# Optimization experiments

Measured on AMD Instinct MI355X. Metric: run time of the kernel, lower is better.

Reference implementation:

```python
import jax, jax.numpy as jnp
import numpy as np

B, CK, CQ, CV, CO, H, W = 4, 256, 256, 256, 64, 24, 24


def setup_inputs() -> dict:
    key = jax.random.key(0)
    ks = jax.random.split(key, 9)
    s = lambda k, shape, fan: jax.random.normal(k, shape, jnp.float32) * (fan ** -0.5)
    return {
        "key": jax.random.normal(ks[0], (B, CK, H, W), jnp.float32),
        "query": jax.random.normal(ks[1], (B, CQ, H, W), jnp.float32),
        "value": jax.random.normal(ks[2], (B, CV, H, W), jnp.float32),
        "Wk": s(ks[3], (CO, CK), CK),   # 1x1 conv weight for key transform
        "bk": jnp.zeros((CO,), jnp.float32),
        "Wq": s(ks[4], (CO, CQ), CQ),   # 1x1 conv weight for query transform
        "bq": jnp.zeros((CO,), jnp.float32),
        "wf": s(ks[5], (CO,), CO),      # channel-flattening 1x1 conv (CO -> 1)
        "bf": jnp.zeros((), jnp.float32),
    }


def reference(key, query, value, Wk, bk, Wq, bq, wf, bf):
    b, _, hq, wq = query.shape
    nk = key.shape[2] * key.shape[3]
    nq = hq * wq
    # 1x1 conv == per-pixel linear; flatten spatial to (B, N, CO)
    k_ = jnp.einsum('bchw,oc->bhwo', key, Wk).reshape(b, nk, -1) + bk
    q_ = jnp.einsum('bchw,oc->bhwo', query, Wq).reshape(b, nq, -1) + bq
    # broadcast add: (B, Nk, 1, CO) + (B, 1, Nq, CO) -> tanh -> reduce channels
    pre = jnp.tanh(k_[:, :, None, :] + q_[:, None, :, :])
    scores = jnp.einsum('bkqc,c->bkq', pre, wf) + bf
    attn = jax.nn.sigmoid(scores)                      # (B, Nk, Nq)
    v_ = value.reshape(b, value.shape[1], nk)          # (B, CV, Nk)
    out = jnp.einsum('bkq,bck->bcq', attn, v_)         # (B, CV, Nq)
    return out.reshape(b, value.shape[1], hq, wq)
```

## Files before the change

kernel.cpp:

```cpp
#include <hip/hip_runtime.h>
#include <hip/hip_bf16.h>

#define BB 4
#define CIN 256
#define CO 64
#define NN 576
#define NKC 18
#define NQT 36

typedef __attribute__((ext_vector_type(8))) short short8;
typedef __attribute__((ext_vector_type(4))) float floatx4;

__device__ __forceinline__ unsigned short f2bf(float f) {
    unsigned int u = __float_as_uint(f);
    unsigned int r = (u + 0x7fffu + ((u >> 16) & 1u)) >> 16;
    return (unsigned short)r;
}

__global__ void transpose_kernel(const float* __restrict__ key,
                                 const float* __restrict__ query,
                                 float* __restrict__ kt,
                                 float* __restrict__ qt) {
    int z = blockIdx.z;
    const float* src = (z < BB) ? key : query;
    float* dst       = (z < BB) ? kt  : qt;
    int b = z & (BB - 1);
    __shared__ float tile[32][33];
    int n0 = blockIdx.x * 32, c0 = blockIdx.y * 32;
    int tx = threadIdx.x, ty = threadIdx.y;
    const float* s = src + (size_t)b * CIN * NN;
    #pragma unroll
    for (int j = 0; j < 4; ++j) {
        int c = c0 + ty + j * 8;
        tile[ty + j * 8][tx] = s[(size_t)c * NN + n0 + tx];
    }
    __syncthreads();
    float* d = dst + (size_t)b * NN * CIN;
    #pragma unroll
    for (int j = 0; j < 4; ++j) {
        int n = n0 + ty + j * 8;
        d[(size_t)n * CIN + c0 + tx] = tile[tx][ty + j * 8];
    }
}

#define NT 4
__global__ void proj_exp_kernel(const float* __restrict__ kt,
                                const float* __restrict__ qt,
                                const float* __restrict__ Wk, const float* __restrict__ bk,
                                const float* __restrict__ Wq, const float* __restrict__ bq,
                                float* __restrict__ ek, float* __restrict__ eq) {
    int z = blockIdx.z;
    const float* xt   = z ? qt : kt;
    const float* W    = z ? Wq : Wk;
    const float* bias = z ? bq : bk;
    float* outp       = z ? eq : ek;
    int b  = blockIdx.y;
    int n0 = blockIdx.x * NT;
    int o  = threadIdx.x;

    float acc[NT];
    float bv = bias[o];
    #pragma unroll
    for (int i = 0; i < NT; ++i) acc[i] = bv;

    const float* wrow  = W + (size_t)o * CIN;
    const float* xbase = xt + ((size_t)b * NN + n0) * CIN;

    for (int c0 = 0; c0 < CIN; c0 += 64) {
        float4 w[16];
        #pragma unroll
        for (int i = 0; i < 16; ++i) w[i] = ((const float4*)(wrow + c0))[i];
        #pragma unroll
        for (int n = 0; n < NT; ++n) {
            const float* xr = xbase + (size_t)n * CIN + c0;
            #pragma unroll
            for (int i = 0; i < 16; ++i) {
                float4 wv = w[i];
                acc[n] = fmaf(wv.x, xr[4 * i + 0], acc[n]);
                acc[n] = fmaf(wv.y, xr[4 * i + 1], acc[n]);
                acc[n] = fmaf(wv.z, xr[4 * i + 2], acc[n]);
                acc[n] = fmaf(wv.w, xr[4 * i + 3], acc[n]);
            }
        }
    }
    float* op = outp + ((size_t)b * NN + n0) * CO + o;
    #pragma unroll
    for (int i = 0; i < NT; ++i) op[(size_t)i * CO] = __expf(2.0f * acc[i]);
}

__global__ void packv_kernel(const float* __restrict__ value,
                             unsigned short* __restrict__ Vp) {
    int ct = blockIdx.x, kc = blockIdx.y, b = blockIdx.z;
    int l = threadIdx.x;
    int c = ct * 16 + (l & 15);
    int k = kc * 32 + (l >> 4) * 8;
    const float4* src = (const float4*)(value + ((size_t)b * CIN + c) * NN + k);
    float4 v0 = src[0], v1 = src[1];
    uint4 o;
    o.x = (unsigned)f2bf(v0.x) | ((unsigned)f2bf(v0.y) << 16);
    o.y = (unsigned)f2bf(v0.z) | ((unsigned)f2bf(v0.w) << 16);
    o.z = (unsigned)f2bf(v1.x) | ((unsigned)f2bf(v1.y) << 16);
    o.w = (unsigned)f2bf(v1.z) | ((unsigned)f2bf(v1.w) << 16);
    *(uint4*)(Vp + (((size_t)b * 16 + ct) * NKC + kc) * 1024 + l * 8) = o;
}

__global__ void __launch_bounds__(256, 3)
attn_pack_kernel(const float* __restrict__ ek,
                 const float* __restrict__ eq,
                 const float* __restrict__ wf,
                 const float* __restrict__ bfp,
                 unsigned short* __restrict__ Bp) {
    int b  = blockIdx.z;
    int k0 = blockIdx.y * 32;
    int q0 = blockIdx.x * 64;
    int t  = threadIdx.x;
    int l  = t & 63;
    int w  = __builtin_amdgcn_readfirstlane(t >> 6);

    float4 eqv[16], w2v[16];
    const float4* eqp = (const float4*)(eq + ((size_t)b * NN + q0 + l) * CO);
    const float4* wfp = (const float4*)wf;
    float C = bfp[0];
    #pragma unroll
    for (int i = 0; i < 16; ++i) {
        eqv[i] = eqp[i];
        float4 wv = wfp[i];
        C += wv.x + wv.y + wv.z + wv.w;
        wv.x *= 2.0f; wv.y *= 2.0f; wv.z *= 2.0f; wv.w *= 2.0f;
        w2v[i] = wv;
    }

    __shared__ float sc[32][64];

    #pragma unroll 1
    for (int kk = 0; kk < 8; ++kk) {
        int k = k0 + w * 8 + kk;
        const float4* ekr = (const float4*)(ek + ((size_t)b * NN + k) * CO);
        float a0 = 0.f, a1 = 0.f, a2 = 0.f, a3 = 0.f;
        #pragma unroll
        for (int i = 0; i < 16; ++i) {
            float4 k4 = ekr[i];
            float4 e4 = eqv[i];
            float4 w4 = w2v[i];
            a0 = fmaf(w4.x, __builtin_amdgcn_rcpf(fmaf(k4.x, e4.x, 1.0f)), a0);
            a1 = fmaf(w4.y, __builtin_amdgcn_rcpf(fmaf(k4.y, e4.y, 1.0f)), a1);
            a2 = fmaf(w4.z, __builtin_amdgcn_rcpf(fmaf(k4.z, e4.z, 1.0f)), a2);
            a3 = fmaf(w4.w, __builtin_amdgcn_rcpf(fmaf(k4.w, e4.w, 1.0f)), a3);
        }
        float score = C - (a0 + a1) - (a2 + a3);
        float sg = __builtin_amdgcn_rcpf(1.0f + __expf(-score));
        sc[w * 8 + kk][l] = sg;
    }
    __syncthreads();

    int col = w * 16 + (l & 15);
    int row = (l >> 4) * 8;
    uint4 o;
    o.x = (unsigned)f2bf(sc[row + 0][col]) | ((unsigned)f2bf(sc[row + 1][col]) << 16);
    o.y = (unsigned)f2bf(sc[row + 2][col]) | ((unsigned)f2bf(sc[row + 3][col]) << 16);
    o.z = (unsigned)f2bf(sc[row + 4][col]) | ((unsigned)f2bf(sc[row + 5][col]) << 16);
    o.w = (unsigned)f2bf(sc[row + 6][col]) | ((unsigned)f2bf(sc[row + 7][col]) << 16);
    size_t qt = (size_t)blockIdx.x * 4 + w;
    *(uint4*)(Bp + (((size_t)b * NQT + qt) * NKC + blockIdx.y) * 1024 + l * 8) = o;
}

__global__ void av_mfma_kernel(const unsigned short* __restrict__ Vp,
                               const unsigned short* __restrict__ Bp,
                               float* __restrict__ out) {
    int b  = blockIdx.z;
    int ct = blockIdx.y;
    int qx = blockIdx.x;
    int t  = threadIdx.x;
    int l  = t & 63;
    int w  = __builtin_amdgcn_readfirstlane(t >> 6);

    floatx4 acc[4] = {{0.f,0.f,0.f,0.f},{0.f,0.f,0.f,0.f},
                      {0.f,0.f,0.f,0.f},{0.f,0.f,0.f,0.f}};

    const unsigned short* abase = Vp + ((size_t)b * 16 + ct) * NKC * 1024 + l * 8;
    const unsigned short* bbase = Bp + ((size_t)b * NQT + (size_t)qx * 4) * NKC * 1024 + l * 8;

    for (int kc = w; kc < NKC; kc += 4) {
        short8 a = *(const short8*)(abase + (size_t)kc * 1024);
        #pragma unroll
        for (int qt = 0; qt < 4; ++qt) {
            short8 bq = *(const short8*)(bbase + ((size_t)qt * NKC + kc) * 1024);
            acc[qt] = __builtin_amdgcn_mfma_f32_16x16x32_bf16(a, bq, acc[qt], 0, 0, 0);
        }
    }

    __shared__ float red[4][64][17];
    #pragma unroll
    for (int qt = 0; qt < 4; ++qt)
        #pragma unroll
        for (int r = 0; r < 4; ++r)
            red[w][l][qt * 4 + r] = acc[qt][r];
    __syncthreads();

    int q = qx * 64 + w * 16 + (l & 15);
    #pragma unroll
    for (int r = 0; r < 4; ++r) {
        float s = red[0][l][w * 4 + r] + red[1][l][w * 4 + r]
                + red[2][l][w * 4 + r] + red[3][l][w * 4 + r];
        int c = ct * 16 + (l >> 4) * 4 + r;
        out[((size_t)b * CIN + c) * NN + q] = s;
    }
}

extern "C" void kernel_launch(void* const* d_in, const int* in_sizes, int n_in,
                              void* d_out, int out_size, void* d_ws, size_t ws_size,
                              hipStream_t stream) {
    const float* key   = (const float*)d_in[0];
    const float* query = (const float*)d_in[1];
    const float* value = (const float*)d_in[2];
    const float* Wk    = (const float*)d_in[3];
    const float* bk    = (const float*)d_in[4];
    const float* Wq    = (const float*)d_in[5];
    const float* bq    = (const float*)d_in[6];
    const float* wf    = (const float*)d_in[7];
    const float* bf    = (const float*)d_in[8];
    float* out = (float*)d_out;

    float* ws = (float*)d_ws;
    float* ek = ws;
    float* eq = ek + (size_t)BB * NN * CO;
    float* bp_region = eq + (size_t)BB * NN * CO;
    unsigned short* Bp = (unsigned short*)bp_region;
    float* kt = bp_region;
    float* qt = kt + (size_t)BB * NN * CIN;
    unsigned short* Vp = (unsigned short*)(bp_region + 1327104);

    dim3 gt(NN / 32, CIN / 32, 2 * BB);
    transpose_kernel<<<gt, dim3(32, 8), 0, stream>>>(key, query, kt, qt);

    dim3 gp(NN / NT, BB, 2);
    proj_exp_kernel<<<gp, 64, 0, stream>>>(kt, qt, Wk, bk, Wq, bq, ek, eq);

    dim3 gv(16, NKC, BB);
    packv_kernel<<<gv, 64, 0, stream>>>(value, Vp);

    dim3 ga(NN / 64, NN / 32, BB);
    attn_pack_kernel<<<ga, 256, 0, stream>>>(ek, eq, wf, bf, Bp);

    dim3 gm(NN / 64, 16, BB);
    av_mfma_kernel<<<gm, 256, 0, stream>>>(Vp, Bp, out);
}
```

Before: 116.8 us.

## Fuse packing kernels and move 1x1 projections onto bf16 MFMA

The separate transpose, value-pack and weight handling steps are merged into one pack_all kernel. It converts key, query, value and both weight matrices to bf16 MFMA fragment layout in a single launch. The scalar fp32 projection kernel is replaced with a bf16 MFMA 16x16x32 GEMM, and the attention kernel now stages eq through padded shared memory with coalesced loads. Packed buffer strides shrink from 1024 to 512 elements, which removes padding waste. The projections lose precision by moving from fp32 to bf16 inputs, and the exp(2x) step can amplify those errors.

```diff
diff --git a/kernel.cpp b/kernel.cpp
--- a/kernel.cpp
+++ b/kernel.cpp
@@ -6,6 +6,7 @@
 #define CO 64
 #define NN 576
 #define NKC 18
+#define NMT 36
 #define NQT 36
 
 typedef __attribute__((ext_vector_type(8))) short short8;
@@ -17,99 +18,127 @@
     return (unsigned short)r;
 }
 
-__global__ void transpose_kernel(const float* __restrict__ key,
-                                 const float* __restrict__ query,
-                                 float* __restrict__ kt,
-                                 float* __restrict__ qt) {
-    int z = blockIdx.z;
-    const float* src = (z < BB) ? key : query;
-    float* dst       = (z < BB) ? kt  : qt;
-    int b = z & (BB - 1);
+__global__ void __launch_bounds__(256) pack_all(
+    const float* __restrict__ key, const float* __restrict__ query,
+    const float* __restrict__ value,
+    const float* __restrict__ Wk, const float* __restrict__ Wq,
+    unsigned short* __restrict__ Xp, unsigned short* __restrict__ Wp,
+    unsigned short* __restrict__ Vp)
+{
     __shared__ float tile[32][33];
-    int n0 = blockIdx.x * 32, c0 = blockIdx.y * 32;
-    int tx = threadIdx.x, ty = threadIdx.y;
-    const float* s = src + (size_t)b * CIN * NN;
-    #pragma unroll
-    for (int j = 0; j < 4; ++j) {
-        int c = c0 + ty + j * 8;
-        tile[ty + j * 8][tx] = s[(size_t)c * NN + n0 + tx];
-    }
-    __syncthreads();
-    float* d = dst + (size_t)b * NN * CIN;
-    #pragma unroll
-    for (int j = 0; j < 4; ++j) {
-        int n = n0 + ty + j * 8;
-        d[(size_t)n * CIN + c0 + tx] = tile[tx][ty + j * 8];
-    }
-}
-
-#define NT 4
-__global__ void proj_exp_kernel(const float* __restrict__ kt,
-                                const float* __restrict__ qt,
-                                const float* __restrict__ Wk, const float* __restrict__ bk,
-                                const float* __restrict__ Wq, const float* __restrict__ bq,
-                                float* __restrict__ ek, float* __restrict__ eq) {
-    int z = blockIdx.z;
-    const float* xt   = z ? qt : kt;
-    const float* W    = z ? Wq : Wk;
+    int bid = blockIdx.x;
+    int t = threadIdx.x;
+    int l = t & 63;
+    int w = t >> 6;
+
+    if (bid < 1152) {
+        int zb  = bid / 144;
+        int r   = bid % 144;
+        int n32 = r % 18;
+        int kc  = r / 18;
+        int z = zb >> 2, b = zb & 3;
+        const float* src = z ? query : key;
+        int tx = t & 31, ty = t >> 5;
+        const float* s = src + ((size_t)b * CIN + (size_t)kc * 32) * NN + n32 * 32;
+        #pragma unroll
+        for (int j = 0; j < 4; ++j) {
+            int cl = ty + j * 8;
+            tile[cl][tx] = s[(size_t)cl * NN + tx];
+        }
+        __syncthreads();
+        if (w < 2) {
+            int nl = w * 16 + (l & 15);
+            int cl = (l >> 4) * 8;
+            uint4 o;
+            o.x = (unsigned)f2bf(tile[cl + 0][nl]) | ((unsigned)f2bf(tile[cl + 1][nl]) << 16);
+            o.y = (unsigned)f2bf(tile[cl + 2][nl]) | ((unsigned)f2bf(tile[cl + 3][nl]) << 16);
+            o.z = (unsigned)f2bf(tile[cl + 4][nl]) | ((unsigned)f2bf(tile[cl + 5][nl]) << 16);
+            o.w = (unsigned)f2bf(tile[cl + 6][nl]) | ((unsigned)f2bf(tile[cl + 7][nl]) << 16);
+            int mt = n32 * 2 + w;
+            *(uint4*)(Xp + ((((size_t)z * BB + b) * NMT + mt) * 8 + kc) * 512 + l * 8) = o;
+        }
+    } else if (bid < 1168) {
+        int funit = (bid - 1152) * 4 + w;
+        int z  = funit >> 5;
+        int nt = (funit >> 3) & 3;
+        int kc = funit & 7;
+        const float* W = z ? Wq : Wk;
+        int o = nt * 16 + (l & 15);
+        int c = kc * 32 + (l >> 4) * 8;
+        const float4* p = (const float4*)(W + (size_t)o * CIN + c);
+        float4 v0 = p[0], v1 = p[1];
+        uint4 u;
+        u.x = (unsigned)f2bf(v0.x) | ((unsigned)f2bf(v0.y) << 16);
+        u.y = (unsigned)f2bf(v0.z) | ((unsigned)f2bf(v0.w) << 16);
+        u.z = (unsigned)f2bf(v1.x) | ((unsigned)f2bf(v1.y) << 16);
+        u.w = (unsigned)f2bf(v1.z) | ((unsigned)f2bf(v1.w) << 16);
+        *(uint4*)(Wp + (((size_t)z * 4 + nt) * 8 + kc) * 512 + l * 8) = u;
+    } else {
+        int funit = (bid - 1168) * 4 + w;
+        int b  = funit / 288;
+        int r  = funit % 288;
+        int ct = r / 18;
+        int kc = r % 18;
+        int c = ct * 16 + (l & 15);
+        int k = kc * 32 + (l >> 4) * 8;
+        const float4* p = (const float4*)(value + ((size_t)b * CIN + c) * NN + k);
+        float4 v0 = p[0], v1 = p[1];
+        uint4 u;
+        u.x = (unsigned)f2bf(v0.x) | ((unsigned)f2bf(v0.y) << 16);
+        u.y = (unsigned)f2bf(v0.z) | ((unsigned)f2bf(v0.w) << 16);
+        u.z = (unsigned)f2bf(v1.x) | ((unsigned)f2bf(v1.y) << 16);
+        u.w = (unsigned)f2bf(v1.z) | ((unsigned)f2bf(v1.w) << 16);
+        *(uint4*)(Vp + (((size_t)b * 16 + ct) * NKC + kc) * 512 + l * 8) = u;
+    }
+}
+
+__global__ void __launch_bounds__(256) proj_exp_mfma(
+    const unsigned short* __restrict__ Xp, const unsigned short* __restrict__ Wp,
+    const float* __restrict__ bk, const float* __restrict__ bq,
+    float* __restrict__ ek, float* __restrict__ eq)
+{
+    int t = threadIdx.x, l = t & 63, w = t >> 6;
+    int gw = blockIdx.x * 4 + w;
+    int z  = gw / 144;
+    int r  = gw % 144;
+    int b  = r / NMT;
+    int mt = r % NMT;
+
+    const unsigned short* ab = Xp + ((((size_t)z * BB + b) * NMT + mt) * 8) * 512 + l * 8;
+    const unsigned short* wb = Wp + (size_t)z * 32 * 512 + l * 8;
+
+    floatx4 acc[4] = {{0.f,0.f,0.f,0.f},{0.f,0.f,0.f,0.f},
+                      {0.f,0.f,0.f,0.f},{0.f,0.f,0.f,0.f}};
+    #pragma unroll
+    for (int kc = 0; kc < 8; ++kc) {
+        short8 a = *(const short8*)(ab + (size_t)kc * 512);
+        #pragma unroll
+        for (int nt = 0; nt < 4; ++nt) {
+            short8 bf8 = *(const short8*)(wb + ((size_t)nt * 8 + kc) * 512);
+            acc[nt] = __builtin_amdgcn_mfma_f32_16x16x32_bf16(a, bf8, acc[nt], 0, 0, 0);
+        }
+    }
+
     const float* bias = z ? bq : bk;
     float* outp       = z ? eq : ek;
-    int b  = blockIdx.y;
-    int n0 = blockIdx.x * NT;
-    int o  = threadIdx.x;
-
-    float acc[NT];
-    float bv = bias[o];
-    #pragma unroll
-    for (int i = 0; i < NT; ++i) acc[i] = bv;
-
-    const float* wrow  = W + (size_t)o * CIN;
-    const float* xbase = xt + ((size_t)b * NN + n0) * CIN;
-
-    for (int c0 = 0; c0 < CIN; c0 += 64) {
-        float4 w[16];
-        #pragma unroll
-        for (int i = 0; i < 16; ++i) w[i] = ((const float4*)(wrow + c0))[i];
-        #pragma unroll
-        for (int n = 0; n < NT; ++n) {
-            const float* xr = xbase + (size_t)n * CIN + c0;
-            #pragma unroll
-            for (int i = 0; i < 16; ++i) {
-                float4 wv = w[i];
-                acc[n] = fmaf(wv.x, xr[4 * i + 0], acc[n]);
-                acc[n] = fmaf(wv.y, xr[4 * i + 1], acc[n]);
-                acc[n] = fmaf(wv.z, xr[4 * i + 2], acc[n]);
-                acc[n] = fmaf(wv.w, xr[4 * i + 3], acc[n]);
-            }
-        }
-    }
-    float* op = outp + ((size_t)b * NN + n0) * CO + o;
-    #pragma unroll
-    for (int i = 0; i < NT; ++i) op[(size_t)i * CO] = __expf(2.0f * acc[i]);
-}
-
-__global__ void packv_kernel(const float* __restrict__ value,
-                             unsigned short* __restrict__ Vp) {
-    int ct = blockIdx.x, kc = blockIdx.y, b = blockIdx.z;
-    int l = threadIdx.x;
-    int c = ct * 16 + (l & 15);
-    int k = kc * 32 + (l >> 4) * 8;
-    const float4* src = (const float4*)(value + ((size_t)b * CIN + c) * NN + k);
-    float4 v0 = src[0], v1 = src[1];
-    uint4 o;
-    o.x = (unsigned)f2bf(v0.x) | ((unsigned)f2bf(v0.y) << 16);
-    o.y = (unsigned)f2bf(v0.z) | ((unsigned)f2bf(v0.w) << 16);
-    o.z = (unsigned)f2bf(v1.x) | ((unsigned)f2bf(v1.y) << 16);
-    o.w = (unsigned)f2bf(v1.z) | ((unsigned)f2bf(v1.w) << 16);
-    *(uint4*)(Vp + (((size_t)b * 16 + ct) * NKC + kc) * 1024 + l * 8) = o;
-}
-
-__global__ void __launch_bounds__(256, 3)
-attn_pack_kernel(const float* __restrict__ ek,
-                 const float* __restrict__ eq,
-                 const float* __restrict__ wf,
-                 const float* __restrict__ bfp,
-                 unsigned short* __restrict__ Bp) {
+    int n0 = mt * 16;
+    #pragma unroll
+    for (int nt = 0; nt < 4; ++nt) {
+        int o = nt * 16 + (l & 15);
+        float bv = bias[o];
+        #pragma unroll
+        for (int rr = 0; rr < 4; ++rr) {
+            int row = (l >> 4) * 4 + rr;
+            outp[((size_t)b * NN + n0 + row) * CO + o] = __expf(2.0f * (acc[nt][rr] + bv));
+        }
+    }
+}
+
+__global__ void __launch_bounds__(256, 3) attn_pack_kernel(
+    const float* __restrict__ ek, const float* __restrict__ eq,
+    const float* __restrict__ wf, const float* __restrict__ bfp,
+    unsigned short* __restrict__ Bp)
+{
     int b  = blockIdx.z;
     int k0 = blockIdx.y * 32;
     int q0 = blockIdx.x * 64;
@@ -117,20 +146,38 @@
     int l  = t & 63;
     int w  = __builtin_amdgcn_readfirstlane(t >> 6);
 
-    float4 eqv[16], w2v[16];
-    const float4* eqp = (const float4*)(eq + ((size_t)b * NN + q0 + l) * CO);
-    const float4* wfp = (const float4*)wf;
+    __shared__ float eqs[64 * 65];
+    __shared__ float sc[32 * 65];
+
+    const float4* esrc = (const float4*)(eq + ((size_t)b * NN + q0) * CO);
+    #pragma unroll
+    for (int i = 0; i < 4; ++i) {
+        int f4  = t + i * 256;
+        int row = f4 >> 4, c4 = (f4 & 15) * 4;
+        float4 v = esrc[f4];
+        int a = row * 65 + c4;
+        eqs[a + 0] = v.x; eqs[a + 1] = v.y; eqs[a + 2] = v.z; eqs[a + 3] = v.w;
+    }
+
+    float4 w2v[16];
     float C = bfp[0];
+    const float4* wfp4 = (const float4*)wf;
     #pragma unroll
     for (int i = 0; i < 16; ++i) {
-        eqv[i] = eqp[i];
-        float4 wv = wfp[i];
+        float4 wv = wfp4[i];
         C += wv.x + wv.y + wv.z + wv.w;
         wv.x *= 2.0f; wv.y *= 2.0f; wv.z *= 2.0f; wv.w *= 2.0f;
         w2v[i] = wv;
     }
-
-    __shared__ float sc[32][64];
+    __syncthreads();
+
+    float4 eqv[16];
+    #pragma unroll
+    for (int i = 0; i < 16; ++i) {
+        int a = l * 65 + i * 4;
+        eqv[i].x = eqs[a]; eqv[i].y = eqs[a + 1];
+        eqv[i].z = eqs[a + 2]; eqv[i].w = eqs[a + 3];
+    }
 
     #pragma unroll 1
     for (int kk = 0; kk < 8; ++kk) {
@@ -149,24 +196,26 @@
         }
         float score = C - (a0 + a1) - (a2 + a3);
         float sg = __builtin_amdgcn_rcpf(1.0f + __expf(-score));
-        sc[w * 8 + kk][l] = sg;
+        sc[(w * 8 + kk) * 65 + l] = sg;
     }
     __syncthreads();
 
     int col = w * 16 + (l & 15);
     int row = (l >> 4) * 8;
     uint4 o;
-    o.x = (unsigned)f2bf(sc[row + 0][col]) | ((unsigned)f2bf(sc[row + 1][col]) << 16);
-    o.y = (unsigned)f2bf(sc[row + 2][col]) | ((unsigned)f2bf(sc[row + 3][col]) << 16);
-    o.z = (unsigned)f2bf(sc[row + 4][col]) | ((unsigned)f2bf(sc[row + 5][col]) << 16);
-    o.w = (unsigned)f2bf(sc[row + 6][col]) | ((unsigned)f2bf(sc[row + 7][col]) << 16);
+    o.x = (unsigned)f2bf(sc[(row + 0) * 65 + col]) | ((unsigned)f2bf(sc[(row + 1) * 65 + col]) << 16);
+    o.y = (unsigned)f2bf(sc[(row + 2) * 65 + col]) | ((unsigned)f2bf(sc[(row + 3) * 65 + col]) << 16);
+    o.z = (unsigned)f2bf(sc[(row + 4) * 65 + col]) | ((unsigned)f2bf(sc[(row + 5) * 65 + col]) << 16);
+    o.w = (unsigned)f2bf(sc[(row + 6) * 65 + col]) | ((unsigned)f2bf(sc[(row + 7) * 65 + col]) << 16);
     size_t qt = (size_t)blockIdx.x * 4 + w;
-    *(uint4*)(Bp + (((size_t)b * NQT + qt) * NKC + blockIdx.y) * 1024 + l * 8) = o;
-}
-
-__global__ void av_mfma_kernel(const unsigned short* __restrict__ Vp,
-                               const unsigned short* __restrict__ Bp,
-                               float* __restrict__ out) {
+    *(uint4*)(Bp + (((size_t)b * NQT + qt) * NKC + blockIdx.y) * 512 + l * 8) = o;
+}
+
+__global__ void __launch_bounds__(256) av_mfma_kernel(
+    const unsigned short* __restrict__ Vp,
+    const unsigned short* __restrict__ Bp,
+    float* __restrict__ out)
+{
     int b  = blockIdx.z;
     int ct = blockIdx.y;
     int qx = blockIdx.x;
@@ -177,14 +226,14 @@
     floatx4 acc[4] = {{0.f,0.f,0.f,0.f},{0.f,0.f,0.f,0.f},
                       {0.f,0.f,0.f,0.f},{0.f,0.f,0.f,0.f}};
 
-    const unsigned short* abase = Vp + ((size_t)b * 16 + ct) * NKC * 1024 + l * 8;
-    const unsigned short* bbase = Bp + ((size_t)b * NQT + (size_t)qx * 4) * NKC * 1024 + l * 8;
+    const unsigned short* abase = Vp + ((size_t)b * 16 + ct) * NKC * 512 + l * 8;
+    const unsigned short* bbase = Bp + ((size_t)b * NQT + (size_t)qx * 4) * NKC * 512 + l * 8;
 
     for (int kc = w; kc < NKC; kc += 4) {
-        short8 a = *(const short8*)(abase + (size_t)kc * 1024);
+        short8 a = *(const short8*)(abase + (size_t)kc * 512);
         #pragma unroll
         for (int qt = 0; qt < 4; ++qt) {
-            short8 bq = *(const short8*)(bbase + ((size_t)qt * NKC + kc) * 1024);
+            short8 bq = *(const short8*)(bbase + ((size_t)qt * NKC + kc) * 512);
             acc[qt] = __builtin_amdgcn_mfma_f32_16x16x32_bf16(a, bq, acc[qt], 0, 0, 0);
         }
     }
@@ -224,20 +273,14 @@
     float* ws = (float*)d_ws;
     float* ek = ws;
     float* eq = ek + (size_t)BB * NN * CO;
-    float* bp_region = eq + (size_t)BB * NN * CO;
-    unsigned short* Bp = (unsigned short*)bp_region;
-    float* kt = bp_region;
-    float* qt = kt + (size_t)BB * NN * CIN;
-    unsigned short* Vp = (unsigned short*)(bp_region + 1327104);
-
-    dim3 gt(NN / 32, CIN / 32, 2 * BB);
-    transpose_kernel<<<gt, dim3(32, 8), 0, stream>>>(key, query, kt, qt);
-
-    dim3 gp(NN / NT, BB, 2);
-    proj_exp_kernel<<<gp, 64, 0, stream>>>(kt, qt, Wk, bk, Wq, bq, ek, eq);
-
-    dim3 gv(16, NKC, BB);
-    packv_kernel<<<gv, 64, 0, stream>>>(value, Vp);
+    unsigned short* Xp = (unsigned short*)(eq + (size_t)BB * NN * CO);
+    unsigned short* Wp = Xp + (size_t)2 * BB * NMT * 8 * 512;
+    unsigned short* Vp = Wp + (size_t)2 * 4 * 8 * 512;
+    unsigned short* Bp = Vp + (size_t)BB * 16 * NKC * 512;
+
+    pack_all<<<1456, 256, 0, stream>>>(key, query, value, Wk, Wq, Xp, Wp, Vp);
+
+    proj_exp_mfma<<<72, 256, 0, stream>>>(Xp, Wp, bk, bq, ek, eq);
 
     dim3 ga(NN / 64, NN / 32, BB);
     attn_pack_kernel<<<ga, 256, 0, stream>>>(ek, eq, wf, bf, Bp);
```

New measurement: 102.3 us. -12.4%, faster.
